# Kernel tuning notes

Measured on AMD Instinct MI355X. Metric: run time of the kernel, lower is better.

Reference implementation:

```python
import jax, jax.numpy as jnp
import numpy as np

N_HEADS = 16
B, T, H, HA = 4, 8192, 1024, 1024

def _split_heads(x, n_heads):
    n, t, d = x.shape
    return x.reshape(n, t, n_heads, d // n_heads).transpose(0, 2, 1, 3)  # [n,h,t,dh]

def setup_inputs() -> dict:
    key = jax.random.key(0)
    ks = jax.random.split(key, 9)
    s = 0.02
    return {
        "q": jax.random.normal(ks[0], (B, T, H), jnp.float32),
        "k": jax.random.normal(ks[1], (B, T, H), jnp.float32),
        "v": jax.random.normal(ks[2], (B, T, H), jnp.float32),
        "mask_q": jnp.ones((B, T), jnp.float32),
        "mask_attn": jnp.ones((B, T), jnp.float32),
        "Wq": jax.random.normal(ks[3], (HA, H), jnp.float32) * s,
        "bq": jnp.zeros((HA,), jnp.float32),
        "Wk": jax.random.normal(ks[4], (HA, H), jnp.float32) * s,
        "bk": jnp.zeros((HA,), jnp.float32),
        "Wv": jax.random.normal(ks[5], (H, H), jnp.float32) * s,
        "bv": jnp.zeros((H,), jnp.float32),
    }

def reference(q, k, v, mask_q, mask_attn, Wq, bq, Wk, bk, Wv, bv):
    # projections (dropout = identity in eval)
    qp = q @ Wq.T + bq
    kp = k @ Wk.T + bk
    vp = v @ Wv.T + bv
    qh = _split_heads(qp, N_HEADS)  # [n,h,t,dqk]
    kh = _split_heads(kp, N_HEADS)
    vh = _split_heads(vp, N_HEADS)  # [n,h,t,dv]
    # additive masking (efficient_attn, outer_attn != 'scaled' branch)
    kh = kh - 10000.0 * (1.0 - mask_attn)[:, None, :, None]
    qh = qh - 10000.0 * (1.0 - mask_q)[:, None, :, None]
    dv = vh.shape[-1]  # d // n_heads where d = hidden (from v)
    # softmax over sequence dim of k, then k^T @ v : [n,h,dqk,dv]
    ctx = jnp.einsum('nhtd,nhte->nhde', jax.nn.softmax(kh, axis=2), vh)
    ctx = ctx / jnp.sqrt(jnp.float32(dv))
    # softmax over feature dim of q, then q @ ctx : [n,h,t,dv]
    out = jnp.einsum('nhtd,nhde->nhte', jax.nn.softmax(qh, axis=-1), ctx)
    n, h, t, e = out.shape
    return out.transpose(0, 2, 1, 3).reshape(n, t, h * e)
```

## Files before the change

kernel.cpp:

```cpp
#include <hip/hip_runtime.h>
#include <hip/hip_bf16.h>
#include <math.h>

#define B_  4
#define T_  8192
#define H_  1024
#define NHEAD 16
#define DH  64
#define BT  (B_*T_)

typedef __attribute__((ext_vector_type(8))) short bf16x8;
typedef __attribute__((ext_vector_type(4))) float f32x4;
typedef __attribute__((ext_vector_type(2))) float f32x2;
typedef __attribute__((ext_vector_type(2))) unsigned short u16x2;
typedef __attribute__((ext_vector_type(4))) unsigned short u16x4;
typedef __attribute__((ext_vector_type(8))) unsigned short u16x8;

static __device__ __forceinline__ float bf2f(unsigned short u) {
  union { unsigned int i; float f; } x; x.i = ((unsigned int)u) << 16; return x.f;
}
static __device__ __forceinline__ unsigned short f2bf(float f) {
  union { float f; unsigned int i; } x; x.f = f;
  unsigned int r = x.i + 0x7fffu + ((x.i >> 16) & 1u);
  return (unsigned short)(r >> 16);
}

#define GL2LDS(gptr, sptr) \
  __builtin_amdgcn_global_load_lds((const __attribute__((address_space(1))) void*)(gptr), \
                                   (__attribute__((address_space(3))) void*)(sptr), 16, 0, 0)

#define BAR() do { asm volatile("" ::: "memory"); __builtin_amdgcn_s_barrier(); \
                   asm volatile("" ::: "memory"); } while (0)

__global__ void cvt_kernel(const float* __restrict__ in, unsigned short* __restrict__ out, int n4) {
  int i = blockIdx.x * blockDim.x + threadIdx.x;
  int stride = gridDim.x * blockDim.x;
  for (int idx = i; idx < n4; idx += stride) {
    float4 v = reinterpret_cast<const float4*>(in)[idx];
    u16x4 o;
    o.x = f2bf(v.x); o.y = f2bf(v.y); o.z = f2bf(v.z); o.w = f2bf(v.w);
    reinterpret_cast<u16x4*>(out)[idx] = o;
  }
}

__global__ __launch_bounds__(512, 2) void gemm256(
    const unsigned short* __restrict__ A,
    const unsigned short* __restrict__ Bm,
    const float* __restrict__ bias,
    unsigned short* __restrict__ C) {
  const int K = 1024, N = 1024;
  __shared__ char lds[131072];
  const int tid = threadIdx.x, lane = tid & 63, wid = tid >> 6;
  const int orig = blockIdx.x;
  const int swzb = (orig & 7) * 64 + (orig >> 3);
  const int bm = (swzb >> 2) * 256, bn = (swzb & 3) * 256;
  const int wm = wid >> 2, wn = wid & 3;

  const int sr   = wid * 8 + (lane >> 3);
  const int scol = ((lane & 7) * 8) ^ ((lane >> 3) << 3);
  const unsigned short* gA = A  + (size_t)(bm + sr) * K + scol;
  const unsigned short* gB = Bm + (size_t)(bn + sr) * K + scol;
  const int dstw = wid * 1024;

  const int aswz  = (lane & 7) << 4;
  const int arow0 = (wm * 128 + (lane & 15)) * 128;
  const int brow0 = 32768 + (wn * 64 + (lane & 15)) * 128;

  f32x4 acc[8][4];
#pragma unroll
  for (int fn = 0; fn < 4; ++fn) {
    float bv = bias[bn + wn * 64 + fn * 16 + (lane & 15)];
    f32x4 sp = {bv, bv, bv, bv};
#pragma unroll
    for (int fm = 0; fm < 8; ++fm) acc[fm][fn] = sp;
  }

  bf16x8 aF[4][2], bF[4][2];

  auto stA4 = [&](int buf, int kt) {
    char* d = lds + buf * 65536 + dstw;
    const unsigned short* g = gA + kt * 64;
    GL2LDS(g, d);
    GL2LDS(g + (size_t)64  * K, d + 8192);
    GL2LDS(g + (size_t)128 * K, d + 16384);
    GL2LDS(g + (size_t)192 * K, d + 24576);
  };
  auto stB = [&](int buf, int kt) {
    char* d = lds + buf * 65536 + 32768 + dstw;
    const unsigned short* g = gB + kt * 64;
    GL2LDS(g, d);
    GL2LDS(g + (size_t)64  * K, d + 8192);
    GL2LDS(g + (size_t)128 * K, d + 16384);
    GL2LDS(g + (size_t)192 * K, d + 24576);
  };
  auto loadA = [&](int buf, int mh) {
#pragma unroll
    for (int f = 0; f < 4; ++f)
#pragma unroll
      for (int ks = 0; ks < 2; ++ks)
        aF[f][ks] = *(const bf16x8*)(lds + buf * 65536 + arow0 + (mh * 4 + f) * 2048
                                     + (((lane >> 4) * 16 + ks * 64) ^ aswz));
  };
  auto loadB = [&](int buf, int nh) {
#pragma unroll
    for (int f = 0; f < 2; ++f)
#pragma unroll
      for (int ks = 0; ks < 2; ++ks)
        bF[nh * 2 + f][ks] = *(const bf16x8*)(lds + buf * 65536 + brow0 + (nh * 2 + f) * 2048
                                              + (((lane >> 4) * 16 + ks * 64) ^ aswz));
  };
  auto quad = [&](int mh, int nh) {
    __builtin_amdgcn_s_setprio(1);
#pragma unroll
    for (int f = 0; f < 4; ++f)
#pragma unroll
      for (int g2 = 0; g2 < 2; ++g2)
#pragma unroll
        for (int ks = 0; ks < 2; ++ks)
          acc[mh * 4 + f][nh * 2 + g2] = __builtin_amdgcn_mfma_f32_16x16x32_bf16(
              aF[f][ks], bF[nh * 2 + g2][ks], acc[mh * 4 + f][nh * 2 + g2], 0, 0, 0);
    __builtin_amdgcn_s_setprio(0);
  };

  stA4(0, 0); stB(0, 0);
  stA4(1, 1); stB(1, 1);
  asm volatile("s_waitcnt vmcnt(8)" ::: "memory");
  BAR();

#define KTILE(t, STG, WSTR, DOW)                              \
  {                                                           \
    const int b_ = (t) & 1;                                   \
    loadA(b_, 0); loadB(b_, 0);                               \
    quad(0, 0);                                               \
    BAR();                                                    \
    loadB(b_, 1);                                             \
    quad(0, 1);                                               \
    BAR();                                                    \
    if (STG) stB(b_, (t) + 2);                                \
    loadA(b_, 1);                                             \
    quad(1, 0);                                               \
    BAR();                                                    \
    if (STG) stA4(b_, (t) + 2);                               \
    quad(1, 1);                                               \
    if (DOW) { asm volatile("s_waitcnt vmcnt(" WSTR ")" ::: "memory"); } \
    BAR();                                                    \
  }

  for (int t = 0; t < 14; ++t) KTILE(t, 1, "8", 1)
  KTILE(14, 0, "0", 1)
  KTILE(15, 0, "0", 0)
#undef KTILE

  const int crow0 = bm + wm * 128 + (lane >> 4) * 4;
  const int ccol0 = bn + wn * 64 + (lane & 15);
#pragma unroll
  for (int fm = 0; fm < 8; ++fm)
#pragma unroll
    for (int j = 0; j < 4; ++j) {
      unsigned short* cp = C + (size_t)(crow0 + fm * 16 + j) * N + ccol0;
#pragma unroll
      for (int fn = 0; fn < 4; ++fn) cp[fn * 16] = f2bf(acc[fm][fn][j]);
    }
}

__global__ __launch_bounds__(256, 2) void phase1(
    const unsigned short* __restrict__ Pk,
    const unsigned short* __restrict__ Pv,
    const float* __restrict__ mask_attn,
    float* __restrict__ Upart,
    float* __restrict__ cspart) {
  const int chunk = blockIdx.x;
  const int nh = blockIdx.y;
  const int n = nh >> 4, h = nh & 15;
  const int tid = threadIdx.x, lane = tid & 63, wid = tid >> 6;
  __shared__ __align__(16) unsigned short ekT[64 * 256];
  __shared__ __align__(16) unsigned short vpT[64 * 256];

  f32x4 acc[5];
#pragma unroll
  for (int i = 0; i < 5; ++i) acc[i] = (f32x4){0.f, 0.f, 0.f, 0.f};
  bf16x8 ones;
#pragma unroll
  for (int j = 0; j < 8; ++j) ones[j] = (short)0x3f80;

  const int isV = tid >> 7;
  const int slot0 = tid & 127;
  const unsigned short* src = isV ? Pv : Pk;
  unsigned short* dstT = isV ? vpT : ekT;

  const int arow = wid * 16 + (lane & 15);
  const int aswz = ((arow & 7) ^ ((arow >> 3) & 7)) << 4;

  for (int stage = 0; stage < 4; ++stage) {
    if (stage) __syncthreads();
#pragma unroll
    for (int r = 0; r < 2; ++r) {
      const int slot = slot0 + r * 128;
      const int toct = slot >> 3;
      const int d0   = (slot & 7) * 8;
      const int tbase = chunk * 1024 + stage * 256 + toct * 8;
      u16x8 in[8];
#pragma unroll
      for (int s = 0; s < 8; ++s)
        in[s] = *(const u16x8*)(src + (size_t)(n * T_ + tbase + s) * H_ + h * DH + d0);
      if (!isV) {
#pragma unroll
        for (int s = 0; s < 8; ++s) {
          const float madd = -10000.f * (1.f - mask_attn[n * T_ + tbase + s]);
          u16x8 o;
#pragma unroll
          for (int j = 0; j < 8; ++j) o[j] = f2bf(__expf(bf2f(in[s][j]) + madd));
          in[s] = o;
        }
      }
#pragma unroll
      for (int i = 0; i < 8; ++i) {
        u16x8 o;
#pragma unroll
        for (int s = 0; s < 8; ++s) o[s] = in[s][i];
        const int d = d0 + i;
        const int boff = (toct * 16) ^ (((d & 7) ^ ((d >> 3) & 7)) << 4);
        *(u16x8*)((char*)dstT + d * 512 + boff) = o;
      }
    }
    __syncthreads();
#pragma unroll
    for (int kk = 0; kk < 8; ++kk) {
      const int koff = kk * 64 + (lane >> 4) * 16;
      bf16x8 af = *(const bf16x8*)((const char*)ekT + arow * 512 + (koff ^ aswz));
      acc[4] = __builtin_amdgcn_mfma_f32_16x16x32_bf16(af, ones, acc[4], 0, 0, 0);
#pragma unroll
      for (int nn = 0; nn < 4; ++nn) {
        const int brow = nn * 16 + (lane & 15);
        const int bswz = ((brow & 7) ^ ((brow >> 3) & 7)) << 4;
        bf16x8 bf_ = *(const bf16x8*)((const char*)vpT + brow * 512 + (koff ^ bswz));
        acc[nn] = __builtin_amdgcn_mfma_f32_16x16x32_bf16(af, bf_, acc[nn], 0, 0, 0);
      }
    }
  }

  const int d = wid * 16 + (lane >> 4) * 4;
  const int e = lane & 15;
  float* up = Upart + ((size_t)(chunk * 64 + nh) * 64) * 64;
#pragma unroll
  for (int nn = 0; nn < 4; ++nn)
#pragma unroll
    for (int j = 0; j < 4; ++j)
      up[(size_t)(d + j) * 64 + nn * 16 + e] = acc[nn][j];
  if (e == 0)
#pragma unroll
    for (int j = 0; j < 4; ++j)
      cspart[((size_t)chunk * 64 + nh) * 64 + d + j] = acc[4][j];
}

__global__ void ctxbuild(const float* __restrict__ Upart,
                         const float* __restrict__ cspart,
                         unsigned short* __restrict__ ctxT) {
  const int nh = blockIdx.x, tid = threadIdx.x;
  __shared__ float cs[64];
  if (tid < 64) {
    float s = 0;
    for (int c = 0; c < 8; ++c) s += cspart[((size_t)c * 64 + nh) * 64 + tid];
    cs[tid] = s;
  }
  __syncthreads();
  const int d0 = (tid >> 4) * 4, e0 = (tid & 15) * 4;
#pragma unroll
  for (int i = 0; i < 4; ++i) {
    const float inv = 0.125f / cs[d0 + i];
#pragma unroll
    for (int j = 0; j < 4; ++j) {
      float s = 0;
      for (int c = 0; c < 8; ++c)
        s += Upart[((size_t)(c * 64 + nh) * 64 + d0 + i) * 64 + e0 + j];
      ctxT[((size_t)nh * 64 + (e0 + j)) * 64 + (d0 + i)] = f2bf(s * inv);
    }
  }
}

__global__ __launch_bounds__(256) void outk(
    const unsigned short* __restrict__ Pq,
    const unsigned short* __restrict__ ctxT,
    float* __restrict__ Out) {
  const int tb = blockIdx.x;
  const int nh = blockIdx.y;
  const int n = nh >> 4, h = nh & 15;
  const int tid = threadIdx.x, lane = tid & 63, wid = tid >> 6;
  __shared__ unsigned short sp[128][72];

  bf16x8 breg[2][4];
#pragma unroll
  for (int ks = 0; ks < 2; ++ks)
#pragma unroll
    for (int nn = 0; nn < 4; ++nn)
      breg[ks][nn] = *(const bf16x8*)(ctxT + ((size_t)nh * 64 + nn * 16 + (lane & 15)) * 64
                                      + ks * 32 + (lane >> 4) * 8);

  const int r = tid >> 1, half = tid & 1;
  const int t0 = tb * 128;
  const size_t qoff = (size_t)(n * T_ + t0 + r) * H_ + h * DH + half * 32;
  u16x8 qv[4];
#pragma unroll
  for (int s = 0; s < 4; ++s) qv[s] = *(const u16x8*)(Pq + qoff + s * 8);
  float e[32]; float sum = 0.f;
#pragma unroll
  for (int s = 0; s < 4; ++s)
#pragma unroll
    for (int j = 0; j < 8; ++j) { float x = __expf(bf2f(qv[s][j])); e[s * 8 + j] = x; sum += x; }
  sum += __shfl_xor(sum, 1);
  const float inv = 1.f / sum;
#pragma unroll
  for (int s = 0; s < 4; ++s) {
    u16x8 pb;
#pragma unroll
    for (int j = 0; j < 8; ++j) pb[j] = f2bf(e[s * 8 + j] * inv);
    *(u16x8*)&sp[r][half * 32 + s * 8] = pb;
  }
  __syncthreads();

  f32x4 acc[2][4];
  f32x4 z = {0.f, 0.f, 0.f, 0.f};
#pragma unroll
  for (int mm = 0; mm < 2; ++mm)
#pragma unroll
    for (int nn = 0; nn < 4; ++nn) acc[mm][nn] = z;
  const int wm = wid * 32;
#pragma unroll
  for (int ks = 0; ks < 2; ++ks) {
    bf16x8 av[2];
#pragma unroll
    for (int mm = 0; mm < 2; ++mm)
      av[mm] = *(const bf16x8*)((const char*)&sp[0][0]
               + (wm + mm * 16 + (lane & 15)) * 144 + ks * 64 + (lane >> 4) * 16);
#pragma unroll
    for (int mm = 0; mm < 2; ++mm)
#pragma unroll
      for (int nn = 0; nn < 4; ++nn)
        acc[mm][nn] = __builtin_amdgcn_mfma_f32_16x16x32_bf16(av[mm], breg[ks][nn], acc[mm][nn], 0, 0, 0);
  }

#pragma unroll
  for (int mm = 0; mm < 2; ++mm)
#pragma unroll
    for (int j = 0; j < 4; ++j) {
      const int row = t0 + wm + mm * 16 + (lane >> 4) * 4 + j;
      float* op = Out + ((size_t)n * T_ + row) * H_ + h * DH + (lane & 15);
#pragma unroll
      for (int nn = 0; nn < 4; ++nn) op[nn * 16] = acc[mm][nn][j];
    }
}

extern "C" void kernel_launch(void* const* d_in, const int* in_sizes, int n_in,
                              void* d_out, int out_size, void* d_ws, size_t ws_size,
                              hipStream_t stream) {
  const float* q  = (const float*)d_in[0];
  const float* k  = (const float*)d_in[1];
  const float* v  = (const float*)d_in[2];
  const float* mask_attn = (const float*)d_in[4];
  const float* Wq = (const float*)d_in[5];
  const float* bq = (const float*)d_in[6];
  const float* Wk = (const float*)d_in[7];
  const float* bk = (const float*)d_in[8];
  const float* Wv = (const float*)d_in[9];
  const float* bv = (const float*)d_in[10];
  float* out = (float*)d_out;

  char* ws = (char*)d_ws;
  size_t off = 0;
  unsigned short* Xb = (unsigned short*)(ws + off); off += (size_t)BT * H_ * 2;
  unsigned short* Wb = (unsigned short*)(ws + off); off += (size_t)3 * H_ * H_ * 2;
  unsigned short* Pq = (unsigned short*)(ws + off); off += (size_t)BT * H_ * 2;
  unsigned short* Pk = (unsigned short*)(ws + off); off += (size_t)BT * H_ * 2;
  unsigned short* Pv = (unsigned short*)(ws + off); off += (size_t)BT * H_ * 2;
  float* Upart  = (float*)(ws + off); off += (size_t)8 * 64 * 64 * 64 * 4;
  float* cspart = (float*)(ws + off); off += (size_t)8 * 64 * 64 * 4;
  unsigned short* ctxT = (unsigned short*)(ws + off); off += (size_t)64 * 64 * 64 * 2;

  dim3 blk(256);
  const int nW4 = H_ * H_ / 4;
  cvt_kernel<<<dim3(512), blk, 0, stream>>>(Wq, Wb + 0 * H_ * H_, nW4);
  cvt_kernel<<<dim3(512), blk, 0, stream>>>(Wk, Wb + 1 * H_ * H_, nW4);
  cvt_kernel<<<dim3(512), blk, 0, stream>>>(Wv, Wb + 2 * H_ * H_, nW4);

  const int nX4 = BT * H_ / 4;
  dim3 gblk(512);
  dim3 ggrid(512);
  cvt_kernel<<<dim3(2048), blk, 0, stream>>>(k, Xb, nX4);
  gemm256<<<ggrid, gblk, 0, stream>>>(Xb, Wb + 1 * H_ * H_, bk, Pk);
  cvt_kernel<<<dim3(2048), blk, 0, stream>>>(v, Xb, nX4);
  gemm256<<<ggrid, gblk, 0, stream>>>(Xb, Wb + 2 * H_ * H_, bv, Pv);
  cvt_kernel<<<dim3(2048), blk, 0, stream>>>(q, Xb, nX4);
  gemm256<<<ggrid, gblk, 0, stream>>>(Xb, Wb + 0 * H_ * H_, bq, Pq);

  phase1<<<dim3(8, 64), blk, 0, stream>>>(Pk, Pv, mask_attn, Upart, cspart);
  ctxbuild<<<dim3(64), blk, 0, stream>>>(Upart, cspart, ctxT);
  outk<<<dim3(64, 64), blk, 0, stream>>>(Pq, ctxT, out);
}
```

Measured before the change: 410.5 us.

## Fuse fp32-to-bf16 activation conversion into GEMM A-tile loading

```diff
diff --git a/kernel.cpp b/kernel.cpp
--- a/kernel.cpp
+++ b/kernel.cpp
@@ -44,7 +44,7 @@
 }
 
 __global__ __launch_bounds__(512, 2) void gemm256(
-    const unsigned short* __restrict__ A,
+    const float* __restrict__ A,
     const unsigned short* __restrict__ Bm,
     const float* __restrict__ bias,
     unsigned short* __restrict__ C) {
@@ -56,9 +56,13 @@
   const int bm = (swzb >> 2) * 256, bn = (swzb & 3) * 256;
   const int wm = wid >> 2, wn = wid & 3;
 
+  const int asr = wid * 8 + (lane >> 3);
+  const int ac0 = (lane & 7) * 8;
+  const float* gA32 = A + (size_t)(bm + asr) * K + ac0;
+  const int awr = asr * 128 + (((lane & 7) * 16) ^ ((asr & 7) << 4));
+
   const int sr   = wid * 8 + (lane >> 3);
   const int scol = ((lane & 7) * 8) ^ ((lane >> 3) << 3);
-  const unsigned short* gA = A  + (size_t)(bm + sr) * K + scol;
   const unsigned short* gB = Bm + (size_t)(bn + sr) * K + scol;
   const int dstw = wid * 1024;
 
@@ -76,14 +80,24 @@
   }
 
   bf16x8 aF[4][2], bF[4][2];
-
-  auto stA4 = [&](int buf, int kt) {
-    char* d = lds + buf * 65536 + dstw;
-    const unsigned short* g = gA + kt * 64;
-    GL2LDS(g, d);
-    GL2LDS(g + (size_t)64  * K, d + 8192);
-    GL2LDS(g + (size_t)128 * K, d + 16384);
-    GL2LDS(g + (size_t)192 * K, d + 24576);
+  f32x4 ar[4][2];
+
+  auto issueA32 = [&](int kt) {
+#pragma unroll
+    for (int s = 0; s < 4; ++s) {
+      const float* g = gA32 + (size_t)(s * 64) * K + kt * 64;
+      ar[s][0] = *(const f32x4*)(g);
+      ar[s][1] = *(const f32x4*)(g + 4);
+    }
+  };
+  auto writeA = [&](int buf) {
+#pragma unroll
+    for (int s = 0; s < 4; ++s) {
+      u16x8 o;
+#pragma unroll
+      for (int j = 0; j < 4; ++j) { o[j] = (short)f2bf(ar[s][0][j]); o[4 + j] = (short)f2bf(ar[s][1][j]); }
+      *(u16x8*)(lds + buf * 65536 + s * 8192 + awr) = o;
+    }
   };
   auto stB = [&](int buf, int kt) {
     char* d = lds + buf * 65536 + 32768 + dstw;
@@ -122,14 +136,21 @@
     __builtin_amdgcn_s_setprio(0);
   };
 
-  stA4(0, 0); stB(0, 0);
-  stA4(1, 1); stB(1, 1);
+  issueA32(0);
+  asm volatile("s_waitcnt vmcnt(0)" ::: "memory");
+  writeA(0);
+  issueA32(1);
+  stB(0, 0); stB(1, 1);
   asm volatile("s_waitcnt vmcnt(8)" ::: "memory");
+  writeA(1);
+  asm volatile("s_waitcnt lgkmcnt(0)" ::: "memory");
+  asm volatile("s_waitcnt vmcnt(4)" ::: "memory");
   BAR();
 
 #define KTILE(t, STG, WSTR, DOW)                              \
   {                                                           \
     const int b_ = (t) & 1;                                   \
+    if (STG) issueA32((t) + 2);                               \
     loadA(b_, 0); loadB(b_, 0);                               \
     quad(0, 0);                                               \
     BAR();                                                    \
@@ -140,13 +161,14 @@
     loadA(b_, 1);                                             \
     quad(1, 0);                                               \
     BAR();                                                    \
-    if (STG) stA4(b_, (t) + 2);                               \
+    if (DOW) { asm volatile("s_waitcnt vmcnt(" WSTR ")" ::: "memory"); } \
+    if (STG) writeA(b_);                                      \
     quad(1, 1);                                               \
-    if (DOW) { asm volatile("s_waitcnt vmcnt(" WSTR ")" ::: "memory"); } \
+    asm volatile("s_waitcnt lgkmcnt(0)" ::: "memory");        \
     BAR();                                                    \
   }
 
-  for (int t = 0; t < 14; ++t) KTILE(t, 1, "8", 1)
+  for (int t = 0; t < 14; ++t) KTILE(t, 1, "4", 1)
   KTILE(14, 0, "0", 1)
   KTILE(15, 0, "0", 0)
 #undef KTILE
@@ -367,7 +389,6 @@
 
   char* ws = (char*)d_ws;
   size_t off = 0;
-  unsigned short* Xb = (unsigned short*)(ws + off); off += (size_t)BT * H_ * 2;
   unsigned short* Wb = (unsigned short*)(ws + off); off += (size_t)3 * H_ * H_ * 2;
   unsigned short* Pq = (unsigned short*)(ws + off); off += (size_t)BT * H_ * 2;
   unsigned short* Pk = (unsigned short*)(ws + off); off += (size_t)BT * H_ * 2;
@@ -382,15 +403,11 @@
   cvt_kernel<<<dim3(512), blk, 0, stream>>>(Wk, Wb + 1 * H_ * H_, nW4);
   cvt_kernel<<<dim3(512), blk, 0, stream>>>(Wv, Wb + 2 * H_ * H_, nW4);
 
-  const int nX4 = BT * H_ / 4;
   dim3 gblk(512);
   dim3 ggrid(512);
-  cvt_kernel<<<dim3(2048), blk, 0, stream>>>(k, Xb, nX4);
-  gemm256<<<ggrid, gblk, 0, stream>>>(Xb, Wb + 1 * H_ * H_, bk, Pk);
-  cvt_kernel<<<dim3(2048), blk, 0, stream>>>(v, Xb, nX4);
-  gemm256<<<ggrid, gblk, 0, stream>>>(Xb, Wb + 2 * H_ * H_, bv, Pv);
-  cvt_kernel<<<dim3(2048), blk, 0, stream>>>(q, Xb, nX4);
-  gemm256<<<ggrid, gblk, 0, stream>>>(Xb, Wb + 0 * H_ * H_, bq, Pq);
+  gemm256<<<ggrid, gblk, 0, stream>>>(k, Wb + 1 * H_ * H_, bk, Pk);
+  gemm256<<<ggrid, gblk, 0, stream>>>(v, Wb + 2 * H_ * H_, bv, Pv);
+  gemm256<<<ggrid, gblk, 0, stream>>>(q, Wb + 0 * H_ * H_, bq, Pq);
 
   phase1<<<dim3(8, 64), blk, 0, stream>>>(Pk, Pv, mask_attn, Upart, cspart);
   ctxbuild<<<dim3(64), blk, 0, stream>>>(Upart, cspart, ctxT);
```

New measurement: 404.7 us. No clear change (-1.4%).

## Fuse fp32-to-bf16 activation conversion into projection GEMM operand loads

Applied to the files above, without the earlier changes.

```diff
diff --git a/kernel.cpp b/kernel.cpp
--- a/kernel.cpp
+++ b/kernel.cpp
@@ -43,28 +43,34 @@
   }
 }
 
-__global__ __launch_bounds__(512, 2) void gemm256(
-    const unsigned short* __restrict__ A,
+__global__ __launch_bounds__(512, 2) void gemm256d(
+    const float* __restrict__ A,
     const unsigned short* __restrict__ Bm,
     const float* __restrict__ bias,
     unsigned short* __restrict__ C) {
   const int K = 1024, N = 1024;
-  __shared__ char lds[131072];
+  __shared__ char lds[98304];
   const int tid = threadIdx.x, lane = tid & 63, wid = tid >> 6;
   const int orig = blockIdx.x;
   const int swzb = (orig & 7) * 64 + (orig >> 3);
   const int bm = (swzb >> 2) * 256, bn = (swzb & 3) * 256;
   const int wm = wid >> 2, wn = wid & 3;
 
-  const int sr   = wid * 8 + (lane >> 3);
-  const int scol = ((lane & 7) * 8) ^ ((lane >> 3) << 3);
-  const unsigned short* gA = A  + (size_t)(bm + sr) * K + scol;
-  const unsigned short* gB = Bm + (size_t)(bn + sr) * K + scol;
+  const int srA   = wid * 8 + (lane >> 3);
+  const int scolA = ((lane & 7) * 4) ^ (((lane >> 3) & 7) << 2);
+  const float* gA = A + (size_t)(bm + srA) * K + scolA;
+
+  const int srB   = wid * 16 + (lane >> 2);
+  const int scolB = ((lane & 3) * 8) ^ (((lane >> 3) & 3) << 3);
+  const unsigned short* gB = Bm + (size_t)(bn + srB) * K + scolB;
   const int dstw = wid * 1024;
 
-  const int aswz  = (lane & 7) << 4;
+  const int aswzA = (lane & 7) << 4;
   const int arow0 = (wm * 128 + (lane & 15)) * 128;
-  const int brow0 = 32768 + (wn * 64 + (lane & 15)) * 128;
+  const int acol0 = (lane >> 4) * 32;
+  const int bswz  = (((lane & 15) >> 1) & 3) << 4;
+  const int brow0 = 32768 + (wn * 64 + (lane & 15)) * 64;
+  const int kcB   = ((lane >> 4) * 16) ^ bswz;
 
   f32x4 acc[8][4];
 #pragma unroll
@@ -75,81 +81,66 @@
     for (int fm = 0; fm < 8; ++fm) acc[fm][fn] = sp;
   }
 
-  bf16x8 aF[4][2], bF[4][2];
-
-  auto stA4 = [&](int buf, int kt) {
-    char* d = lds + buf * 65536 + dstw;
-    const unsigned short* g = gA + kt * 64;
-    GL2LDS(g, d);
-    GL2LDS(g + (size_t)64  * K, d + 8192);
-    GL2LDS(g + (size_t)128 * K, d + 16384);
-    GL2LDS(g + (size_t)192 * K, d + 24576);
+  bf16x8 bF[4];
+
+  auto stA = [&](int buf, int kt) {
+    char* d = lds + buf * 49152 + dstw;
+    const float* g = gA + kt * 32;
+#pragma unroll
+    for (int gg = 0; gg < 4; ++gg)
+      GL2LDS(g + (size_t)(gg * 64) * K, d + gg * 8192);
   };
   auto stB = [&](int buf, int kt) {
-    char* d = lds + buf * 65536 + 32768 + dstw;
-    const unsigned short* g = gB + kt * 64;
+    char* d = lds + buf * 49152 + 32768 + dstw;
+    const unsigned short* g = gB + kt * 32;
     GL2LDS(g, d);
-    GL2LDS(g + (size_t)64  * K, d + 8192);
-    GL2LDS(g + (size_t)128 * K, d + 16384);
-    GL2LDS(g + (size_t)192 * K, d + 24576);
+    GL2LDS(g + (size_t)128 * K, d + 8192);
   };
-  auto loadA = [&](int buf, int mh) {
-#pragma unroll
-    for (int f = 0; f < 4; ++f)
-#pragma unroll
-      for (int ks = 0; ks < 2; ++ks)
-        aF[f][ks] = *(const bf16x8*)(lds + buf * 65536 + arow0 + (mh * 4 + f) * 2048
-                                     + (((lane >> 4) * 16 + ks * 64) ^ aswz));
+  auto loadB4 = [&](int buf) {
+#pragma unroll
+    for (int n = 0; n < 4; ++n)
+      bF[n] = *(const bf16x8*)(lds + buf * 49152 + brow0 + n * 1024 + kcB);
   };
-  auto loadB = [&](int buf, int nh) {
-#pragma unroll
-    for (int f = 0; f < 2; ++f)
-#pragma unroll
-      for (int ks = 0; ks < 2; ++ks)
-        bF[nh * 2 + f][ks] = *(const bf16x8*)(lds + buf * 65536 + brow0 + (nh * 2 + f) * 2048
-                                              + (((lane >> 4) * 16 + ks * 64) ^ aswz));
+  auto loadAcvt = [&](int buf, int f) -> bf16x8 {
+    const char* p = lds + buf * 49152 + arow0 + f * 2048;
+    f32x4 lo = *(const f32x4*)(p + (acol0 ^ aswzA));
+    f32x4 hi = *(const f32x4*)(p + ((acol0 + 16) ^ aswzA));
+    union { unsigned int u[4]; bf16x8 v; } cv;
+    asm("v_cvt_pk_bf16_f32 %0, %1, %2" : "=v"(cv.u[0]) : "v"(lo[0]), "v"(lo[1]));
+    asm("v_cvt_pk_bf16_f32 %0, %1, %2" : "=v"(cv.u[1]) : "v"(lo[2]), "v"(lo[3]));
+    asm("v_cvt_pk_bf16_f32 %0, %1, %2" : "=v"(cv.u[2]) : "v"(hi[0]), "v"(hi[1]));
+    asm("v_cvt_pk_bf16_f32 %0, %1, %2" : "=v"(cv.u[3]) : "v"(hi[2]), "v"(hi[3]));
+    return cv.v;
   };
-  auto quad = [&](int mh, int nh) {
-    __builtin_amdgcn_s_setprio(1);
-#pragma unroll
-    for (int f = 0; f < 4; ++f)
-#pragma unroll
-      for (int g2 = 0; g2 < 2; ++g2)
-#pragma unroll
-        for (int ks = 0; ks < 2; ++ks)
-          acc[mh * 4 + f][nh * 2 + g2] = __builtin_amdgcn_mfma_f32_16x16x32_bf16(
-              aF[f][ks], bF[nh * 2 + g2][ks], acc[mh * 4 + f][nh * 2 + g2], 0, 0, 0);
-    __builtin_amdgcn_s_setprio(0);
-  };
-
-  stA4(0, 0); stB(0, 0);
-  stA4(1, 1); stB(1, 1);
-  asm volatile("s_waitcnt vmcnt(8)" ::: "memory");
+
+  stA(0, 0); stB(0, 0);
+  stA(1, 1); stB(1, 1);
+  asm volatile("s_waitcnt vmcnt(6)" ::: "memory");
   BAR();
 
-#define KTILE(t, STG, WSTR, DOW)                              \
+#define KT(t, STG, DOW, WSTR)                                 \
   {                                                           \
     const int b_ = (t) & 1;                                   \
-    loadA(b_, 0); loadB(b_, 0);                               \
-    quad(0, 0);                                               \
+    loadB4(b_);                                               \
+    _Pragma("unroll")                                         \
+    for (int f = 0; f < 8; ++f) {                             \
+      bf16x8 aF = loadAcvt(b_, f);                            \
+      __builtin_amdgcn_s_setprio(1);                          \
+      _Pragma("unroll")                                       \
+      for (int n = 0; n < 4; ++n)                             \
+        acc[f][n] = __builtin_amdgcn_mfma_f32_16x16x32_bf16(aF, bF[n], acc[f][n], 0, 0, 0); \
+      __builtin_amdgcn_s_setprio(0);                          \
+    }                                                         \
     BAR();                                                    \
-    loadB(b_, 1);                                             \
-    quad(0, 1);                                               \
-    BAR();                                                    \
-    if (STG) stB(b_, (t) + 2);                                \
-    loadA(b_, 1);                                             \
-    quad(1, 0);                                               \
-    BAR();                                                    \
-    if (STG) stA4(b_, (t) + 2);                               \
-    quad(1, 1);                                               \
+    if (STG) { stA(b_, (t) + 2); stB(b_, (t) + 2); }          \
     if (DOW) { asm volatile("s_waitcnt vmcnt(" WSTR ")" ::: "memory"); } \
     BAR();                                                    \
   }
 
-  for (int t = 0; t < 14; ++t) KTILE(t, 1, "8", 1)
-  KTILE(14, 0, "0", 1)
-  KTILE(15, 0, "0", 0)
-#undef KTILE
+  for (int t = 0; t < 30; ++t) KT(t, 1, 1, "6")
+  KT(30, 0, 1, "0")
+  KT(31, 0, 0, "0")
+#undef KT
 
   const int crow0 = bm + wm * 128 + (lane >> 4) * 4;
   const int ccol0 = bn + wn * 64 + (lane & 15);
@@ -367,7 +358,6 @@
 
   char* ws = (char*)d_ws;
   size_t off = 0;
-  unsigned short* Xb = (unsigned short*)(ws + off); off += (size_t)BT * H_ * 2;
   unsigned short* Wb = (unsigned short*)(ws + off); off += (size_t)3 * H_ * H_ * 2;
   unsigned short* Pq = (unsigned short*)(ws + off); off += (size_t)BT * H_ * 2;
   unsigned short* Pk = (unsigned short*)(ws + off); off += (size_t)BT * H_ * 2;
@@ -382,15 +372,11 @@
   cvt_kernel<<<dim3(512), blk, 0, stream>>>(Wk, Wb + 1 * H_ * H_, nW4);
   cvt_kernel<<<dim3(512), blk, 0, stream>>>(Wv, Wb + 2 * H_ * H_, nW4);
 
-  const int nX4 = BT * H_ / 4;
   dim3 gblk(512);
   dim3 ggrid(512);
-  cvt_kernel<<<dim3(2048), blk, 0, stream>>>(k, Xb, nX4);
-  gemm256<<<ggrid, gblk, 0, stream>>>(Xb, Wb + 1 * H_ * H_, bk, Pk);
-  cvt_kernel<<<dim3(2048), blk, 0, stream>>>(v, Xb, nX4);
-  gemm256<<<ggrid, gblk, 0, stream>>>(Xb, Wb + 2 * H_ * H_, bv, Pv);
-  cvt_kernel<<<dim3(2048), blk, 0, stream>>>(q, Xb, nX4);
-  gemm256<<<ggrid, gblk, 0, stream>>>(Xb, Wb + 0 * H_ * H_, bq, Pq);
+  gemm256d<<<ggrid, gblk, 0, stream>>>(k, Wb + 1 * H_ * H_, bk, Pk);
+  gemm256d<<<ggrid, gblk, 0, stream>>>(v, Wb + 2 * H_ * H_, bv, Pv);
+  gemm256d<<<ggrid, gblk, 0, stream>>>(q, Wb + 0 * H_ * H_, bq, Pq);
 
   phase1<<<dim3(8, 64), blk, 0, stream>>>(Pk, Pv, mask_attn, Upart, cspart);
   ctxbuild<<<dim3(64), blk, 0, stream>>>(Upart, cspart, ctxT);
```

After: 414.8 us. Within noise of the previous version (+1.0%).

## Restructure GEMM main loop into 8-phase half-tile staged pipeline

Applied to the files above, without the earlier changes.

```diff
diff --git a/kernel.cpp b/kernel.cpp
--- a/kernel.cpp
+++ b/kernel.cpp
@@ -77,21 +77,17 @@
 
   bf16x8 aF[4][2], bF[4][2];
 
-  auto stA4 = [&](int buf, int kt) {
-    char* d = lds + buf * 65536 + dstw;
-    const unsigned short* g = gA + kt * 64;
+  auto stHA = [&](int buf, int kt, int h) {
+    char* d = lds + buf * 65536 + h * 16384 + dstw;
+    const unsigned short* g = gA + (size_t)(h * 128) * K + kt * 64;
     GL2LDS(g, d);
-    GL2LDS(g + (size_t)64  * K, d + 8192);
-    GL2LDS(g + (size_t)128 * K, d + 16384);
-    GL2LDS(g + (size_t)192 * K, d + 24576);
+    GL2LDS(g + (size_t)64 * K, d + 8192);
   };
-  auto stB = [&](int buf, int kt) {
-    char* d = lds + buf * 65536 + 32768 + dstw;
-    const unsigned short* g = gB + kt * 64;
+  auto stHB = [&](int buf, int kt, int h) {
+    char* d = lds + buf * 65536 + 32768 + h * 16384 + dstw;
+    const unsigned short* g = gB + (size_t)(h * 128) * K + kt * 64;
     GL2LDS(g, d);
-    GL2LDS(g + (size_t)64  * K, d + 8192);
-    GL2LDS(g + (size_t)128 * K, d + 16384);
-    GL2LDS(g + (size_t)192 * K, d + 24576);
+    GL2LDS(g + (size_t)64 * K, d + 8192);
   };
   auto loadA = [&](int buf, int mh) {
 #pragma unroll
@@ -101,13 +97,13 @@
         aF[f][ks] = *(const bf16x8*)(lds + buf * 65536 + arow0 + (mh * 4 + f) * 2048
                                      + (((lane >> 4) * 16 + ks * 64) ^ aswz));
   };
-  auto loadB = [&](int buf, int nh) {
-#pragma unroll
-    for (int f = 0; f < 2; ++f)
+  auto loadB2 = [&](int buf, int nh) {
+#pragma unroll
+    for (int g2 = 0; g2 < 2; ++g2)
 #pragma unroll
       for (int ks = 0; ks < 2; ++ks)
-        bF[nh * 2 + f][ks] = *(const bf16x8*)(lds + buf * 65536 + brow0 + (nh * 2 + f) * 2048
-                                              + (((lane >> 4) * 16 + ks * 64) ^ aswz));
+        bF[nh * 2 + g2][ks] = *(const bf16x8*)(lds + buf * 65536 + brow0 + (nh * 2 + g2) * 2048
+                                               + (((lane >> 4) * 16 + ks * 64) ^ aswz));
   };
   auto quad = [&](int mh, int nh) {
     __builtin_amdgcn_s_setprio(1);
@@ -122,34 +118,44 @@
     __builtin_amdgcn_s_setprio(0);
   };
 
-  stA4(0, 0); stB(0, 0);
-  stA4(1, 1); stB(1, 1);
-  asm volatile("s_waitcnt vmcnt(8)" ::: "memory");
+#define PHASE(READS, STAGE, LGKM8, DOVM, VMSTR, MH, NH)       \
+  {                                                           \
+    READS;                                                    \
+    STAGE;                                                    \
+    if (LGKM8) asm volatile("s_waitcnt lgkmcnt(8)" ::: "memory"); \
+    BAR();                                                    \
+    asm volatile("s_waitcnt lgkmcnt(0)" ::: "memory");        \
+    __builtin_amdgcn_sched_barrier(0);                        \
+    quad(MH, NH);                                             \
+    if (DOVM) asm volatile("s_waitcnt vmcnt(" VMSTR ")" ::: "memory"); \
+    BAR();                                                    \
+  }
+
+  stHA(0, 0, 0); stHA(0, 0, 1); stHB(0, 0, 0); stHB(0, 0, 1);
+  stHB(1, 1, 0); stHA(1, 1, 0);
+  asm volatile("s_waitcnt vmcnt(4)" ::: "memory");
   BAR();
 
-#define KTILE(t, STG, WSTR, DOW)                              \
-  {                                                           \
-    const int b_ = (t) & 1;                                   \
-    loadA(b_, 0); loadB(b_, 0);                               \
-    quad(0, 0);                                               \
-    BAR();                                                    \
-    loadB(b_, 1);                                             \
-    quad(0, 1);                                               \
-    BAR();                                                    \
-    if (STG) stB(b_, (t) + 2);                                \
-    loadA(b_, 1);                                             \
-    quad(1, 0);                                               \
-    BAR();                                                    \
-    if (STG) stA4(b_, (t) + 2);                               \
-    quad(1, 1);                                               \
-    if (DOW) { asm volatile("s_waitcnt vmcnt(" WSTR ")" ::: "memory"); } \
-    BAR();                                                    \
-  }
-
-  for (int t = 0; t < 14; ++t) KTILE(t, 1, "8", 1)
-  KTILE(14, 0, "0", 1)
-  KTILE(15, 0, "0", 0)
-#undef KTILE
+  for (int it = 0; it < 7; ++it) {
+    const int t0 = 2 * it;
+    PHASE(loadA(0, 0); loadB2(0, 0), stHA(1, t0 + 1, 1), 1, 0, "4", 0, 0)
+    PHASE(loadB2(0, 1),              stHB(1, t0 + 1, 1), 0, 0, "4", 0, 1)
+    PHASE(loadA(0, 1),               stHB(0, t0 + 2, 0), 0, 0, "4", 1, 1)
+    PHASE((void)0,                   stHA(0, t0 + 2, 0), 0, 1, "4", 1, 0)
+    PHASE(loadA(1, 0); loadB2(1, 0), stHA(0, t0 + 2, 1), 1, 0, "4", 0, 0)
+    PHASE(loadB2(1, 1),              stHB(0, t0 + 2, 1), 0, 0, "4", 0, 1)
+    PHASE(loadA(1, 1),               stHB(1, t0 + 3, 0), 0, 0, "4", 1, 1)
+    PHASE((void)0,                   stHA(1, t0 + 3, 0), 0, 1, "4", 1, 0)
+  }
+  PHASE(loadA(0, 0); loadB2(0, 0), stHA(1, 15, 1), 1, 0, "4", 0, 0)
+  PHASE(loadB2(0, 1),              stHB(1, 15, 1), 0, 0, "4", 0, 1)
+  PHASE(loadA(0, 1),               (void)0,        0, 0, "4", 1, 1)
+  PHASE((void)0,                   (void)0,        0, 1, "0", 1, 0)
+  PHASE(loadA(1, 0); loadB2(1, 0), (void)0,        1, 0, "4", 0, 0)
+  PHASE(loadB2(1, 1),              (void)0,        0, 0, "4", 0, 1)
+  PHASE(loadA(1, 1),               (void)0,        0, 0, "4", 1, 1)
+  PHASE((void)0,                   (void)0,        0, 0, "4", 1, 0)
+#undef PHASE
 
   const int crow0 = bm + wm * 128 + (lane >> 4) * 4;
   const int ccol0 = bn + wn * 64 + (lane & 15);
```

Result: no change. 405.1 us (-1.3%).
